# Optimization experiments

Measured on AMD Instinct MI355X. Metric: run time of the kernel, lower is better.

Reference implementation:

```python
import jax, jax.numpy as jnp
import numpy as np

D_MODEL = 768
NUM_HEADS = 12
HEAD_DIM = D_MODEL // NUM_HEADS


def setup_inputs() -> dict:
    key = jax.random.key(0)
    ks = jax.random.split(key, 9)
    B, S = 4, 2048
    x = jax.random.normal(ks[0], (B, S, D_MODEL), dtype=jnp.float32)
    y = jax.random.normal(ks[1], (B, S, D_MODEL), dtype=jnp.float32)
    mask = jnp.zeros((1, 1, S, S), dtype=jnp.float32)
    s = 1.0 / np.sqrt(D_MODEL)
    Wq = jax.random.normal(ks[2], (D_MODEL, D_MODEL), dtype=jnp.float32) * s
    bq = jnp.zeros((D_MODEL,), dtype=jnp.float32)
    Wkv = jax.random.normal(ks[3], (2 * D_MODEL, D_MODEL), dtype=jnp.float32) * s
    bkv = jnp.zeros((2 * D_MODEL,), dtype=jnp.float32)
    Wo = jax.random.normal(ks[4], (D_MODEL, D_MODEL), dtype=jnp.float32) * s
    bo = jnp.zeros((D_MODEL,), dtype=jnp.float32)
    return {"x": x, "y": y, "mask": mask, "Wq": Wq, "bq": bq,
            "Wkv": Wkv, "bkv": bkv, "Wo": Wo, "bo": bo}


def reference(x, y, mask, Wq, bq, Wkv, bkv, Wo, bo):
    B, S, _ = x.shape
    H, Dh = NUM_HEADS, HEAD_DIM
    # q = Linear(x); kv = Linear(y)   (torch Linear: x @ W.T + b)
    q = x @ Wq.T + bq                      # [B, S, D]
    kv = y @ Wkv.T + bkv                   # [B, S, 2D]
    q = q.reshape(B, S, H, Dh).transpose(0, 2, 1, 3)          # [B, H, S, Dh]
    kv = kv.reshape(B, S, H, 2 * Dh).transpose(0, 2, 1, 3)    # [B, H, S, 2Dh]
    k, v = kv[..., :Dh], kv[..., Dh:]
    scaled = jnp.einsum('bhqd,bhkd->bhqk', q, k) / jnp.sqrt(jnp.float32(Dh))
    scaled = scaled + mask
    attn = jax.nn.softmax(scaled, axis=-1)                    # [B, H, S, S]
    values = jnp.einsum('bhqk,bhkd->bhqd', attn, v)           # [B, H, S, Dh]
    values = values.transpose(0, 2, 1, 3).reshape(B, S, H * Dh)
    return values @ Wo.T + bo
```

## Files before the change

kernel.cpp:

```cpp
#include <hip/hip_runtime.h>
#include <cstdint>

#define S_LEN 2048
#define BATCH 4
#define NHEADS 12
#define DHEAD 64
#define DMODEL 768
#define SCALE_LOG2E 0.18033688011112042f
#define LOG2E 1.4426950408889634f

typedef unsigned short ushort_t;
typedef __attribute__((ext_vector_type(8))) __bf16 bf16x8;
typedef __attribute__((ext_vector_type(4))) float floatx4;

__device__ __forceinline__ ushort_t f2bf(float f) {
  unsigned u = __builtin_bit_cast(unsigned, f);
  u += 0x7fffu + ((u >> 16) & 1u);
  return (ushort_t)(u >> 16);
}

#if __has_builtin(__builtin_amdgcn_cvt_pk_bf16_f32)
__device__ __forceinline__ unsigned pk2bf(float a, float b) {
  auto v = __builtin_amdgcn_cvt_pk_bf16_f32(a, b);
  return __builtin_bit_cast(unsigned, v);
}
#else
__device__ __forceinline__ unsigned pk2bf(float a, float b) {
  unsigned ua = __builtin_bit_cast(unsigned, a);
  unsigned ub = __builtin_bit_cast(unsigned, b);
  ua += 0x7fffu + ((ua >> 16) & 1u);
  ub += 0x7fffu + ((ub >> 16) & 1u);
  return __builtin_amdgcn_perm(ub, ua, 0x07060302);
}
#endif

__device__ __forceinline__ float fexp2(float x) {
#if __has_builtin(__builtin_amdgcn_exp2f)
  return __builtin_amdgcn_exp2f(x);
#else
  return exp2f(x);
#endif
}

__device__ __forceinline__ void gld16(const void* g, void* s) {
  __builtin_amdgcn_global_load_lds(
      (const __attribute__((address_space(1))) void*)g,
      (__attribute__((address_space(3))) void*)s, 16, 0, 0);
}

__device__ __forceinline__ floatx4 mfma16(bf16x8 a, bf16x8 b, floatx4 c) {
  return __builtin_amdgcn_mfma_f32_16x16x32_bf16(a, b, c, 0, 0, 0);
}

__global__ void cvt_mask(const float* __restrict__ x, ushort_t* __restrict__ xb,
                         const float* __restrict__ y, ushort_t* __restrict__ yb,
                         const float* __restrict__ wq, ushort_t* __restrict__ wqb,
                         const float* __restrict__ wkv, ushort_t* __restrict__ wkvb,
                         const float* __restrict__ wo, ushort_t* __restrict__ wob,
                         const float* __restrict__ mask, int* __restrict__ flag) {
  int bx = blockIdx.x;
  if (bx >= 14592) {
    int i = (bx - 14592) * 256 + threadIdx.x;
    float4 v = ((const float4*)mask)[i];
    if (v.x != 0.f || v.y != 0.f || v.z != 0.f || v.w != 0.f) *flag = 0;
    return;
  }
  const float* s;
  ushort_t* d;
  int base;
  if (bx < 6144) { s = x; d = xb; base = bx; }
  else if (bx < 12288) { s = y; d = yb; base = bx - 6144; }
  else if (bx < 12864) { s = wq; d = wqb; base = bx - 12288; }
  else if (bx < 14016) { s = wkv; d = wkvb; base = bx - 12864; }
  else { s = wo; d = wob; base = bx - 14016; }
  int i = base * 256 + threadIdx.x;
  float4 v = ((const float4*)s)[i];
  uint2 o;
  o.x = pk2bf(v.x, v.y);
  o.y = pk2bf(v.z, v.w);
  ((uint2*)d)[i] = o;
}

#define GSTAGE(K0, BUF)                                                   \
  {                                                                       \
    gld16(ag + (K0), (char*)As + (BUF)*8192 + (wave << 10));              \
    gld16(ag + (K0) + 64 * K, (char*)As + (BUF)*8192 + (wave << 10) + 4096); \
    gld16(bg + (K0), (char*)Bs + (BUF)*8192 + (wave << 10));              \
    gld16(bg + (K0) + 64 * K, (char*)Bs + (BUF)*8192 + (wave << 10) + 4096); \
  }

__global__ __launch_bounds__(256, 3) void gemm_qkv(
    const ushort_t* __restrict__ xb, const ushort_t* __restrict__ wqb,
    const float* __restrict__ bq, ushort_t* __restrict__ Qh,
    const ushort_t* __restrict__ yb, const ushort_t* __restrict__ wkvb,
    const float* __restrict__ bkv, ushort_t* __restrict__ Kh,
    ushort_t* __restrict__ Vt) {
  __shared__ __align__(16) ushort_t As[2][128 * 32];
  __shared__ __align__(16) ushort_t Bs[2][128 * 32];
  const int tid = threadIdx.x;
  const int wave = tid >> 6, lane = tid & 63;
  const int wm = wave >> 1, wn = wave & 1;
  const bool isQ = blockIdx.x < 6;
  const int bn = (isQ ? blockIdx.x : blockIdx.x - 6) * 128;
  const int bm = blockIdx.y * 128;
  const ushort_t* A = isQ ? xb : yb;
  const ushort_t* W = isQ ? wqb : wkvb;
  const float* bias = isQ ? bq : bkv;
  const int K = DMODEL;
  const int fr = lane & 15, fq = lane >> 4;

  const int rT = tid >> 2;
  const int cT = ((tid & 3) ^ (rT & 3)) << 3;
  const ushort_t* ag = A + (size_t)(bm + rT) * K + cT;
  const ushort_t* bg = W + (size_t)(bn + rT) * K + cT;

  floatx4 acc[4][4] = {};
  GSTAGE(0, 0);
  __syncthreads();
  for (int k0 = 0; k0 < K; k0 += 32) {
    const int cur = (k0 >> 5) & 1;
    if (k0 + 32 < K) GSTAGE(k0 + 32, cur ^ 1);
    const ushort_t* Ac = As[cur];
    const ushort_t* Bc = Bs[cur];
    bf16x8 af[4], bf[4];
#pragma unroll
    for (int i = 0; i < 4; i++)
      af[i] = *(const bf16x8*)(Ac + (wm * 64 + i * 16 + fr) * 32 + ((fq ^ (fr & 3)) << 3));
#pragma unroll
    for (int j = 0; j < 4; j++)
      bf[j] = *(const bf16x8*)(Bc + (wn * 64 + j * 16 + fr) * 32 + ((fq ^ (fr & 3)) << 3));
#pragma unroll
    for (int i = 0; i < 4; i++)
#pragma unroll
      for (int j = 0; j < 4; j++)
        acc[i][j] = mfma16(af[i], bf[j], acc[i][j]);
    __syncthreads();
  }

#pragma unroll
  for (int i = 0; i < 4; i++) {
#pragma unroll
    for (int j = 0; j < 4; j++) {
#pragma unroll
      for (int r = 0; r < 4; r++) {
        int m = bm + wm * 64 + i * 16 + fq * 4 + r;
        int n = bn + wn * 64 + j * 16 + fr;
        float v = acc[i][j][r] + bias[n];
        int b = m >> 11, s = m & 2047;
        if (isQ) {
          int h = n >> 6, d = n & 63;
          Qh[(((size_t)b * NHEADS + h) * S_LEN + s) * DHEAD + d] = f2bf(v * SCALE_LOG2E);
        } else {
          int h = n >> 7, jj = n & 127;
          if (jj < 64) {
            Kh[(((size_t)b * NHEADS + h) * S_LEN + s) * DHEAD + jj] = f2bf(v);
          } else {
            int s6 = s & 63;
            int sp = (s & ~63) | ((s6 & 2) << 4) | (((s6 >> 2) & 3) << 3) |
                     ((s6 & 1) << 2) | (s6 >> 4);
            Vt[(((size_t)b * NHEADS + h) * DHEAD + (jj - 64)) * S_LEN + sp] = f2bf(v);
          }
        }
      }
    }
  }
}

__global__ __launch_bounds__(256, 3) void gemm_out(
    const ushort_t* __restrict__ A, const ushort_t* __restrict__ W,
    const float* __restrict__ bias, float* __restrict__ o32) {
  __shared__ __align__(16) ushort_t As[2][128 * 32];
  __shared__ __align__(16) ushort_t Bs[2][128 * 32];
  const int tid = threadIdx.x;
  const int wave = tid >> 6, lane = tid & 63;
  const int wm = wave >> 1, wn = wave & 1;
  const int bm = blockIdx.y * 128, bn = blockIdx.x * 128;
  const int K = DMODEL;
  const int fr = lane & 15, fq = lane >> 4;

  const int rT = tid >> 2;
  const int cT = ((tid & 3) ^ (rT & 3)) << 3;
  const ushort_t* ag = A + (size_t)(bm + rT) * K + cT;
  const ushort_t* bg = W + (size_t)(bn + rT) * K + cT;

  floatx4 acc[4][4] = {};
  GSTAGE(0, 0);
  __syncthreads();
  for (int k0 = 0; k0 < K; k0 += 32) {
    const int cur = (k0 >> 5) & 1;
    if (k0 + 32 < K) GSTAGE(k0 + 32, cur ^ 1);
    const ushort_t* Ac = As[cur];
    const ushort_t* Bc = Bs[cur];
    bf16x8 af[4], bf[4];
#pragma unroll
    for (int i = 0; i < 4; i++)
      af[i] = *(const bf16x8*)(Ac + (wm * 64 + i * 16 + fr) * 32 + ((fq ^ (fr & 3)) << 3));
#pragma unroll
    for (int j = 0; j < 4; j++)
      bf[j] = *(const bf16x8*)(Bc + (wn * 64 + j * 16 + fr) * 32 + ((fq ^ (fr & 3)) << 3));
#pragma unroll
    for (int i = 0; i < 4; i++)
#pragma unroll
      for (int j = 0; j < 4; j++)
        acc[i][j] = mfma16(af[i], bf[j], acc[i][j]);
    __syncthreads();
  }

#pragma unroll
  for (int i = 0; i < 4; i++)
#pragma unroll
    for (int j = 0; j < 4; j++)
#pragma unroll
      for (int r = 0; r < 4; r++) {
        int m = bm + wm * 64 + i * 16 + fq * 4 + r;
        int n = bn + wn * 64 + j * 16 + fr;
        o32[(size_t)m * DMODEL + n] = acc[i][j][r] + bias[n];
      }
}

__global__ __launch_bounds__(256, 3) void flash_attn(
    const ushort_t* __restrict__ Qh, const ushort_t* __restrict__ Kh,
    const ushort_t* __restrict__ Vt, const float* __restrict__ mask,
    const int* __restrict__ mask_is_zero, ushort_t* __restrict__ Oh) {
  __shared__ __align__(16) ushort_t Ks[2][64 * 64];
  __shared__ __align__(16) ushort_t Vs[2][64 * 64];
  const int g = blockIdx.x;
  const int qt = (g >> 3) & 15;
  const int bh = ((g >> 7) << 3) | (g & 7);
  const int b = bh / NHEADS, h = bh % NHEADS;
  const int tid = threadIdx.x, w = tid >> 6, lane = tid & 63;
  const int li = lane & 15, lg = lane >> 4, sx = li & 7;
  const bool use_mask = (*mask_is_zero == 0);

  const int q0 = qt * 128 + w * 32;
  const ushort_t* qg = Qh + ((size_t)bh * S_LEN + q0) * DHEAD;
  bf16x8 qf[2][2];
#pragma unroll
  for (int m = 0; m < 2; m++)
#pragma unroll
    for (int kk = 0; kk < 2; kk++)
      qf[m][kk] = *(const bf16x8*)(qg + (m * 16 + li) * 64 + kk * 32 + lg * 8);

  const int srow = lane >> 3;
  const int schk = (lane & 7) ^ srow;
  const ushort_t* kg = Kh + (size_t)bh * S_LEN * DHEAD;
  const ushort_t* vg = Vt + (size_t)bh * DHEAD * S_LEN;

  float m_i[2], l_pq[2];
  floatx4 o_accT[4][2] = {};
#pragma unroll
  for (int m = 0; m < 2; m++) { m_i[m] = -1e30f; l_pq[m] = 0.f; }

#define STAGE(KT, BUF)                                                            \
  {                                                                               \
    const ushort_t* k0_ = kg + (size_t)((KT)*64 + w * 16 + srow) * 64 + schk * 8; \
    gld16(k0_, (char*)Ks + (BUF)*8192 + w * 2048);                                \
    gld16(k0_ + 8 * 64, (char*)Ks + (BUF)*8192 + w * 2048 + 1024);                \
    const ushort_t* v0_ = vg + (size_t)(w * 16 + srow) * 2048 + (KT)*64 + schk * 8; \
    gld16(v0_, (char*)Vs + (BUF)*8192 + w * 2048);                                \
    gld16(v0_ + 8 * 2048, (char*)Vs + (BUF)*8192 + w * 2048 + 1024);              \
  }

  STAGE(0, 0);
  __syncthreads();

  for (int kt = 0; kt < S_LEN / 64; kt++) {
    const int cur = kt & 1;
    if (kt < S_LEN / 64 - 1) STAGE(kt + 1, cur ^ 1);
    const ushort_t* Kc = Ks[cur];
    const ushort_t* Vc = Vs[cur];

    floatx4 sc[2][4];
#pragma unroll
    for (int c = 0; c < 4; c++) {
      bf16x8 kf0 = *(const bf16x8*)(Kc + (c * 16 + li) * 64 + ((lg ^ sx) << 3));
      bf16x8 kf1 = *(const bf16x8*)(Kc + (c * 16 + li) * 64 + (((4 + lg) ^ sx) << 3));
#pragma unroll
      for (int m = 0; m < 2; m++) {
        floatx4 s = {};
        s = mfma16(kf0, qf[m][0], s);
        s = mfma16(kf1, qf[m][1], s);
        sc[m][c] = s;
      }
    }

    bf16x8 pf[2][2];
    if (!use_mask) {
#pragma unroll
      for (int m = 0; m < 2; m++) {
        float cs[4];
#pragma unroll
        for (int c = 0; c < 4; c++) {
          float e0 = fexp2(sc[m][c][0]);
          float e1 = fexp2(sc[m][c][1]);
          float e2 = fexp2(sc[m][c][2]);
          float e3 = fexp2(sc[m][c][3]);
          sc[m][c][0] = e0; sc[m][c][1] = e1; sc[m][c][2] = e2; sc[m][c][3] = e3;
          cs[c] = (e0 + e1) + (e2 + e3);
        }
        l_pq[m] += (cs[0] + cs[1]) + (cs[2] + cs[3]);
      }
    } else {
#pragma unroll
      for (int m = 0; m < 2; m++) {
        int q = q0 + m * 16 + li;
#pragma unroll
        for (int c = 0; c < 4; c++) {
          float4 mv = *(const float4*)(mask + (size_t)q * S_LEN + kt * 64 + c * 16 + lg * 4);
          sc[m][c][0] += mv.x * LOG2E;
          sc[m][c][1] += mv.y * LOG2E;
          sc[m][c][2] += mv.z * LOG2E;
          sc[m][c][3] += mv.w * LOG2E;
        }
        float mx = sc[m][0][0];
#pragma unroll
        for (int c = 0; c < 4; c++)
#pragma unroll
          for (int r = 0; r < 4; r++) mx = fmaxf(mx, sc[m][c][r]);
        mx = fmaxf(mx, __shfl_xor(mx, 16));
        mx = fmaxf(mx, __shfl_xor(mx, 32));
        float mn = fmaxf(m_i[m], mx);
        float al = fexp2(m_i[m] - mn);
        m_i[m] = mn;
        float cs[4];
#pragma unroll
        for (int c = 0; c < 4; c++) {
          float e0 = fexp2(sc[m][c][0] - mn);
          float e1 = fexp2(sc[m][c][1] - mn);
          float e2 = fexp2(sc[m][c][2] - mn);
          float e3 = fexp2(sc[m][c][3] - mn);
          sc[m][c][0] = e0; sc[m][c][1] = e1; sc[m][c][2] = e2; sc[m][c][3] = e3;
          cs[c] = (e0 + e1) + (e2 + e3);
        }
        l_pq[m] = l_pq[m] * al + (cs[0] + cs[1]) + (cs[2] + cs[3]);
#pragma unroll
        for (int dt = 0; dt < 4; dt++)
#pragma unroll
          for (int r = 0; r < 4; r++) o_accT[dt][m][r] *= al;
      }
    }

#pragma unroll
    for (int m = 0; m < 2; m++)
#pragma unroll
      for (int kk = 0; kk < 2; kk++) {
        uint4 u;
        u.x = pk2bf(sc[m][0][2 * kk], sc[m][1][2 * kk]);
        u.y = pk2bf(sc[m][2][2 * kk], sc[m][3][2 * kk]);
        u.z = pk2bf(sc[m][0][2 * kk + 1], sc[m][1][2 * kk + 1]);
        u.w = pk2bf(sc[m][2][2 * kk + 1], sc[m][3][2 * kk + 1]);
        pf[m][kk] = __builtin_bit_cast(bf16x8, u);
      }

#pragma unroll
    for (int kk = 0; kk < 2; kk++)
#pragma unroll
      for (int dt = 0; dt < 4; dt++) {
        bf16x8 vf = *(const bf16x8*)(Vc + (dt * 16 + li) * 64 + (((kk * 4 + lg) ^ sx) << 3));
#pragma unroll
        for (int m = 0; m < 2; m++) o_accT[dt][m] = mfma16(vf, pf[m][kk], o_accT[dt][m]);
      }
    __syncthreads();
  }

#pragma unroll
  for (int m = 0; m < 2; m++) {
    float l = l_pq[m];
    l += __shfl_xor(l, 16);
    l += __shfl_xor(l, 32);
    float inv = 1.0f / l;
    int q = q0 + m * 16 + li;
    ushort_t* ob = Oh + ((size_t)b * S_LEN + q) * DMODEL + h * DHEAD + lg * 4;
#pragma unroll
    for (int dt = 0; dt < 4; dt++) {
      uint2 pv;
      pv.x = pk2bf(o_accT[dt][m][0] * inv, o_accT[dt][m][1] * inv);
      pv.y = pk2bf(o_accT[dt][m][2] * inv, o_accT[dt][m][3] * inv);
      *(uint2*)(ob + dt * 16) = pv;
    }
  }
}

extern "C" void kernel_launch(void* const* d_in, const int* in_sizes, int n_in,
                              void* d_out, int out_size, void* d_ws, size_t ws_size,
                              hipStream_t stream) {
  const float* x = (const float*)d_in[0];
  const float* y = (const float*)d_in[1];
  const float* mask = (const float*)d_in[2];
  const float* Wq = (const float*)d_in[3];
  const float* bq = (const float*)d_in[4];
  const float* Wkv = (const float*)d_in[5];
  const float* bkv = (const float*)d_in[6];
  const float* Wo = (const float*)d_in[7];
  const float* bo = (const float*)d_in[8];
  float* out = (float*)d_out;

  ushort_t* ws = (ushort_t*)d_ws;
  const size_t XN = (size_t)BATCH * S_LEN * DMODEL;
  ushort_t* xb = ws;
  ushort_t* yb = xb + XN;
  ushort_t* wqb = yb + XN;
  ushort_t* wkvb = wqb + (size_t)DMODEL * DMODEL;
  ushort_t* wob = wkvb + (size_t)2 * DMODEL * DMODEL;
  ushort_t* Qh = wob + (size_t)DMODEL * DMODEL;
  ushort_t* Kh = Qh + XN;
  ushort_t* Vt = Kh + XN;
  int* flag = (int*)(Vt + XN);
  ushort_t* Oh = xb;

  hipMemsetAsync(flag, 1, 4, stream);
  cvt_mask<<<18688, 256, 0, stream>>>(x, xb, y, yb, Wq, wqb, Wkv, wkvb, Wo, wob,
                                      mask, flag);
  gemm_qkv<<<dim3(18, 64), 256, 0, stream>>>(xb, wqb, bq, Qh, yb, wkvb, bkv, Kh, Vt);
  flash_attn<<<768, 256, 0, stream>>>(Qh, Kh, Vt, mask, flag, Oh);
  gemm_out<<<dim3(6, 64), 256, 0, stream>>>(Oh, wob, bo, out);
}
```

Before: 270.8 us.

## Stage V transpose through LDS, swizzle GEMM grids, shrink output GEMM tile

The QKV GEMM epilogue now writes the V half into shared memory and then emits the transposed Vt tile with coalesced 16-byte stores, replacing scattered 2-byte writes. The P fragment packing in flash attention and the Vt key permutation change together so the new layout stays consistent. Both GEMMs use a 1D grid with a remapped block order, which groups neighbouring tiles across XCDs. The output GEMM uses 64x128 tiles with a higher occupancy hint to produce more blocks. The risks are an extra LDS round trip and barrier in the QKV epilogue, and a layout mismatch if the new permutation is wrong.

```diff
diff --git a/kernel.cpp b/kernel.cpp
--- a/kernel.cpp
+++ b/kernel.cpp
@@ -81,11 +81,11 @@
   ((uint2*)d)[i] = o;
 }
 
-#define GSTAGE(K0, BUF)                                                   \
-  {                                                                       \
-    gld16(ag + (K0), (char*)As + (BUF)*8192 + (wave << 10));              \
+#define GSTAGE(K0, BUF)                                                      \
+  {                                                                          \
+    gld16(ag + (K0), (char*)As + (BUF)*8192 + (wave << 10));                 \
     gld16(ag + (K0) + 64 * K, (char*)As + (BUF)*8192 + (wave << 10) + 4096); \
-    gld16(bg + (K0), (char*)Bs + (BUF)*8192 + (wave << 10));              \
+    gld16(bg + (K0), (char*)Bs + (BUF)*8192 + (wave << 10));                 \
     gld16(bg + (K0) + 64 * K, (char*)Bs + (BUF)*8192 + (wave << 10) + 4096); \
   }
 
@@ -95,14 +95,19 @@
     const ushort_t* __restrict__ yb, const ushort_t* __restrict__ wkvb,
     const float* __restrict__ bkv, ushort_t* __restrict__ Kh,
     ushort_t* __restrict__ Vt) {
-  __shared__ __align__(16) ushort_t As[2][128 * 32];
-  __shared__ __align__(16) ushort_t Bs[2][128 * 32];
+  __shared__ __align__(16) ushort_t smem[2 * 4096 + 2 * 4096];
+  ushort_t* As = smem;
+  ushort_t* Bs = smem + 8192;
   const int tid = threadIdx.x;
   const int wave = tid >> 6, lane = tid & 63;
   const int wm = wave >> 1, wn = wave & 1;
-  const bool isQ = blockIdx.x < 6;
-  const int bn = (isQ ? blockIdx.x : blockIdx.x - 6) * 128;
-  const int bm = blockIdx.y * 128;
+  const int g = blockIdx.x;
+  const int r144 = g >> 3;
+  const int by = (g & 7) * 8 + r144 / 18;
+  const int bxr = r144 % 18;
+  const bool isQ = bxr < 6;
+  const int bn = (isQ ? bxr : bxr - 6) * 128;
+  const int bm = by * 128;
   const ushort_t* A = isQ ? xb : yb;
   const ushort_t* W = isQ ? wqb : wkvb;
   const float* bias = isQ ? bq : bkv;
@@ -120,8 +125,8 @@
   for (int k0 = 0; k0 < K; k0 += 32) {
     const int cur = (k0 >> 5) & 1;
     if (k0 + 32 < K) GSTAGE(k0 + 32, cur ^ 1);
-    const ushort_t* Ac = As[cur];
-    const ushort_t* Bc = Bs[cur];
+    const ushort_t* Ac = As + cur * 4096;
+    const ushort_t* Bc = Bs + cur * 4096;
     bf16x8 af[4], bf[4];
 #pragma unroll
     for (int i = 0; i < 4; i++)
@@ -137,44 +142,80 @@
     __syncthreads();
   }
 
-#pragma unroll
-  for (int i = 0; i < 4; i++) {
-#pragma unroll
-    for (int j = 0; j < 4; j++) {
-#pragma unroll
-      for (int r = 0; r < 4; r++) {
-        int m = bm + wm * 64 + i * 16 + fq * 4 + r;
-        int n = bn + wn * 64 + j * 16 + fr;
-        float v = acc[i][j][r] + bias[n];
-        int b = m >> 11, s = m & 2047;
-        if (isQ) {
-          int h = n >> 6, d = n & 63;
+  const int b = bm >> 11, sloc = bm & 2047;
+  if (isQ) {
+#pragma unroll
+    for (int i = 0; i < 4; i++)
+#pragma unroll
+      for (int j = 0; j < 4; j++)
+#pragma unroll
+        for (int r = 0; r < 4; r++) {
+          int m = bm + wm * 64 + i * 16 + fq * 4 + r;
+          int n = bn + wn * 64 + j * 16 + fr;
+          float v = acc[i][j][r] + bias[n];
+          int s = m & 2047, h = n >> 6, d = n & 63;
           Qh[(((size_t)b * NHEADS + h) * S_LEN + s) * DHEAD + d] = f2bf(v * SCALE_LOG2E);
-        } else {
-          int h = n >> 7, jj = n & 127;
-          if (jj < 64) {
+        }
+  } else {
+    const int h = bn >> 7;
+    ushort_t* Vls = smem;
+    if (wn == 0) {
+#pragma unroll
+      for (int i = 0; i < 4; i++)
+#pragma unroll
+        for (int j = 0; j < 4; j++)
+#pragma unroll
+          for (int r = 0; r < 4; r++) {
+            int m = bm + wm * 64 + i * 16 + fq * 4 + r;
+            int n = bn + j * 16 + fr;
+            float v = acc[i][j][r] + bias[n];
+            int s = m & 2047, jj = n & 127;
             Kh[(((size_t)b * NHEADS + h) * S_LEN + s) * DHEAD + jj] = f2bf(v);
-          } else {
-            int s6 = s & 63;
-            int sp = (s & ~63) | ((s6 & 2) << 4) | (((s6 >> 2) & 3) << 3) |
-                     ((s6 & 1) << 2) | (s6 >> 4);
-            Vt[(((size_t)b * NHEADS + h) * DHEAD + (jj - 64)) * S_LEN + sp] = f2bf(v);
           }
+    } else {
+#pragma unroll
+      for (int j = 0; j < 4; j++) {
+        int d = j * 16 + fr;
+        float bv = bias[bn + 64 + j * 16 + fr];
+#pragma unroll
+        for (int i = 0; i < 4; i++) {
+          int m = wm * 64 + i * 16 + fq * 4;
+          uint2 pv;
+          pv.x = pk2bf(acc[i][j][0] + bv, acc[i][j][1] + bv);
+          pv.y = pk2bf(acc[i][j][2] + bv, acc[i][j][3] + bv);
+          *(uint2*)(Vls + d * 132 + m) = pv;
         }
       }
     }
-  }
-}
-
-__global__ __launch_bounds__(256, 3) void gemm_out(
+    __syncthreads();
+    const int dbase = wave * 4 + (lane >> 4);
+    const int blk = (lane >> 3) & 1, oct = lane & 7;
+    const int kbase = blk * 64 + ((oct >> 2) << 5) + ((oct & 3) << 2);
+    ushort_t* vout = Vt + (((size_t)b * NHEADS + h) * DHEAD) * S_LEN + sloc +
+                     blk * 64 + oct * 8;
+#pragma unroll
+    for (int k = 0; k < 4; k++) {
+      int dd = dbase + k * 16;
+      uint2 lo = *(const uint2*)(Vls + dd * 132 + kbase);
+      uint2 hi = *(const uint2*)(Vls + dd * 132 + kbase + 16);
+      uint4 u = {lo.x, lo.y, hi.x, hi.y};
+      *(uint4*)(vout + (size_t)dd * S_LEN) = u;
+    }
+  }
+}
+
+__global__ __launch_bounds__(256, 4) void gemm_out(
     const ushort_t* __restrict__ A, const ushort_t* __restrict__ W,
     const float* __restrict__ bias, float* __restrict__ o32) {
-  __shared__ __align__(16) ushort_t As[2][128 * 32];
+  __shared__ __align__(16) ushort_t As[2][64 * 32];
   __shared__ __align__(16) ushort_t Bs[2][128 * 32];
   const int tid = threadIdx.x;
   const int wave = tid >> 6, lane = tid & 63;
   const int wm = wave >> 1, wn = wave & 1;
-  const int bm = blockIdx.y * 128, bn = blockIdx.x * 128;
+  const int g = blockIdx.x;
+  const int r96 = g >> 3;
+  const int bm = ((g & 7) * 16 + r96 / 6) * 64;
+  const int bn = (r96 % 6) * 128;
   const int K = DMODEL;
   const int fr = lane & 15, fq = lane >> 4;
 
@@ -183,23 +224,30 @@
   const ushort_t* ag = A + (size_t)(bm + rT) * K + cT;
   const ushort_t* bg = W + (size_t)(bn + rT) * K + cT;
 
-  floatx4 acc[4][4] = {};
-  GSTAGE(0, 0);
+#define GOSTAGE(K0, BUF)                                                     \
+  {                                                                          \
+    gld16(ag + (K0), (char*)As + (BUF)*4096 + (wave << 10));                 \
+    gld16(bg + (K0), (char*)Bs + (BUF)*8192 + (wave << 10));                 \
+    gld16(bg + (K0) + 64 * K, (char*)Bs + (BUF)*8192 + (wave << 10) + 4096); \
+  }
+
+  floatx4 acc[2][4] = {};
+  GOSTAGE(0, 0);
   __syncthreads();
   for (int k0 = 0; k0 < K; k0 += 32) {
     const int cur = (k0 >> 5) & 1;
-    if (k0 + 32 < K) GSTAGE(k0 + 32, cur ^ 1);
-    const ushort_t* Ac = As[cur];
-    const ushort_t* Bc = Bs[cur];
-    bf16x8 af[4], bf[4];
-#pragma unroll
-    for (int i = 0; i < 4; i++)
-      af[i] = *(const bf16x8*)(Ac + (wm * 64 + i * 16 + fr) * 32 + ((fq ^ (fr & 3)) << 3));
+    if (k0 + 32 < K) GOSTAGE(k0 + 32, cur ^ 1);
+    const ushort_t* Ac = (const ushort_t*)As + cur * 2048;
+    const ushort_t* Bc = (const ushort_t*)Bs + cur * 4096;
+    bf16x8 af[2], bf[4];
+#pragma unroll
+    for (int i = 0; i < 2; i++)
+      af[i] = *(const bf16x8*)(Ac + (wm * 32 + i * 16 + fr) * 32 + ((fq ^ (fr & 3)) << 3));
 #pragma unroll
     for (int j = 0; j < 4; j++)
       bf[j] = *(const bf16x8*)(Bc + (wn * 64 + j * 16 + fr) * 32 + ((fq ^ (fr & 3)) << 3));
 #pragma unroll
-    for (int i = 0; i < 4; i++)
+    for (int i = 0; i < 2; i++)
 #pragma unroll
       for (int j = 0; j < 4; j++)
         acc[i][j] = mfma16(af[i], bf[j], acc[i][j]);
@@ -207,12 +255,12 @@
   }
 
 #pragma unroll
-  for (int i = 0; i < 4; i++)
+  for (int i = 0; i < 2; i++)
 #pragma unroll
     for (int j = 0; j < 4; j++)
 #pragma unroll
       for (int r = 0; r < 4; r++) {
-        int m = bm + wm * 64 + i * 16 + fq * 4 + r;
+        int m = bm + wm * 32 + i * 16 + fq * 4 + r;
         int n = bn + wn * 64 + j * 16 + fr;
         o32[(size_t)m * DMODEL + n] = acc[i][j][r] + bias[n];
       }
@@ -284,7 +332,6 @@
       }
     }
 
-    bf16x8 pf[2][2];
     if (!use_mask) {
 #pragma unroll
       for (int m = 0; m < 2; m++) {
@@ -340,15 +387,16 @@
       }
     }
 
+    bf16x8 pf[2][2];
 #pragma unroll
     for (int m = 0; m < 2; m++)
 #pragma unroll
       for (int kk = 0; kk < 2; kk++) {
         uint4 u;
-        u.x = pk2bf(sc[m][0][2 * kk], sc[m][1][2 * kk]);
-        u.y = pk2bf(sc[m][2][2 * kk], sc[m][3][2 * kk]);
-        u.z = pk2bf(sc[m][0][2 * kk + 1], sc[m][1][2 * kk + 1]);
-        u.w = pk2bf(sc[m][2][2 * kk + 1], sc[m][3][2 * kk + 1]);
+        u.x = pk2bf(sc[m][2 * kk][0], sc[m][2 * kk][1]);
+        u.y = pk2bf(sc[m][2 * kk][2], sc[m][2 * kk][3]);
+        u.z = pk2bf(sc[m][2 * kk + 1][0], sc[m][2 * kk + 1][1]);
+        u.w = pk2bf(sc[m][2 * kk + 1][2], sc[m][2 * kk + 1][3]);
         pf[m][kk] = __builtin_bit_cast(bf16x8, u);
       }
 
@@ -411,7 +459,7 @@
   hipMemsetAsync(flag, 1, 4, stream);
   cvt_mask<<<18688, 256, 0, stream>>>(x, xb, y, yb, Wq, wqb, Wkv, wkvb, Wo, wob,
                                       mask, flag);
-  gemm_qkv<<<dim3(18, 64), 256, 0, stream>>>(xb, wqb, bq, Qh, yb, wkvb, bkv, Kh, Vt);
+  gemm_qkv<<<1152, 256, 0, stream>>>(xb, wqb, bq, Qh, yb, wkvb, bkv, Kh, Vt);
   flash_attn<<<768, 256, 0, stream>>>(Qh, Kh, Vt, mask, flag, Oh);
-  gemm_out<<<dim3(6, 64), 256, 0, stream>>>(Oh, wob, bo, out);
-}
+  gemm_out<<<768, 256, 0, stream>>>(Oh, wob, bo, out);
+}
```

Measured after the change: 256.7 us. 5.2% less time.
